# Kernel tuning notes

Measured on AMD Instinct MI355X. Metric: run time of the kernel, lower is better.

Reference implementation:

```python
import jax, jax.numpy as jnp
import numpy as np

N_NODES = 50000
N_EDGES = 800000
F_IN = 128
HID = 128
HID4 = HID // 4  # 32
N_SEL = 8192


def gcn_conv(x, src, dst, norm, W, b, n_nodes):
    h = x @ W                              # [N, out]
    msg = h[src] * norm[:, None]           # gather + scale, [E+N, out]
    out = jax.ops.segment_sum(msg, dst, num_segments=n_nodes)  # scatter-add
    return out + b


def setup_inputs() -> dict:
    key = jax.random.key(0)
    ks = jax.random.split(key, 12)
    def glorot(k, shape):
        lim = np.sqrt(6.0 / (shape[0] + shape[1])).astype(np.float32)
        return jax.random.uniform(k, shape, jnp.float32, -lim, lim)
    return {
        "x": jax.random.normal(ks[0], (N_NODES, F_IN), jnp.float32),
        "edge_index": jax.random.randint(ks[1], (2, N_EDGES), 0, N_NODES, jnp.int64 if jax.config.jax_enable_x64 else jnp.int32),
        "relevant_batch_indices": jax.random.randint(ks[2], (N_SEL,), 0, N_NODES),
        "labels": jax.random.randint(ks[3], (N_SEL,), 0, 2),
        "W1": glorot(ks[4], (F_IN, HID)),   "b1": jnp.zeros((HID,), jnp.float32),
        "W2": glorot(ks[5], (HID, HID4)),   "b2": jnp.zeros((HID4,), jnp.float32),
        "W3": glorot(ks[6], (HID4, HID4)),  "b3": jnp.zeros((HID4,), jnp.float32),
        "Wl": glorot(ks[7], (HID4, 2)),     "bl": jnp.zeros((2,), jnp.float32),
    }


def reference(x, edge_index, relevant_batch_indices, labels, W1, b1, W2, b2, W3, b3, Wl, bl):
    n = x.shape[0]
    loops = jnp.arange(n, dtype=edge_index.dtype)
    src = jnp.concatenate([edge_index[0], loops])  # add self-loops
    dst = jnp.concatenate([edge_index[1], loops])
    deg = jax.ops.segment_sum(jnp.ones_like(dst, dtype=x.dtype), dst, num_segments=n)
    dis = jnp.where(deg > 0, jax.lax.rsqrt(jnp.maximum(deg, 1e-12)), 0.0)
    norm = dis[src] * dis[dst]             # [E+N]

    h = jax.nn.relu(gcn_conv(x, src, dst, norm, W1, b1, n))
    h = jax.nn.relu(gcn_conv(h, src, dst, norm, W2, b2, n))
    h = gcn_conv(h, src, dst, norm, W3, b3, n)

    logits = h[relevant_batch_indices] @ Wl + bl   # [N_SEL, 2]
    softmax_vals = jax.nn.softmax(logits, axis=1)
    lsm = jax.nn.log_softmax(logits, axis=1)
    # original slices lsm to labels length if longer; here shapes match
    lsm = lsm[: labels.shape[0]]
    return (lsm, softmax_vals)
```

## Files before the change

### kernel.cpp

```cpp
#include <hip/hip_runtime.h>
#include <hip/hip_fp16.h>

#define F_IN 128
#define HID 128
#define HID4 32
#define NPB 256
#define SRC_BITS 17
#define NBK 256
#define MAXBUCKET 256

static inline size_t alignup(size_t x) { return (x + 255) & ~(size_t)255; }

typedef _Float16 half8 __attribute__((ext_vector_type(8)));
typedef float f32x4 __attribute__((ext_vector_type(4)));

union F4H8 { float4 f; __half2 h[4]; };
union U2H4 { uint2 u; _Float16 h[4]; };


__global__ __launch_bounds__(1024) void hist_k(const int* __restrict__ dst,
                                               int* __restrict__ ghist,
                                               const float* __restrict__ W1,
                                               _Float16* __restrict__ Wt,
                                               int ne, int n_buckets) {
    __shared__ int h[MAXBUCKET];
    const int t = threadIdx.x;
    if (blockIdx.x < 16) {
        int q = blockIdx.x * 1024 + t;
        int k = q >> 7, n = q & 127;
        Wt[n * 128 + k] = (_Float16)W1[q];
    }
    for (int b = t; b < n_buckets; b += 1024) h[b] = 0;
    __syncthreads();
    const int chunk = (ne + NBK - 1) / NBK;
    const int beg = blockIdx.x * chunk;
    const int end = min(ne, beg + chunk);
    for (int e = beg + t; e < end; e += 1024)
        atomicAdd(&h[dst[e] / NPB], 1);
    __syncthreads();
    for (int b = t; b < n_buckets; b += 1024)
        ghist[(size_t)b * NBK + blockIdx.x] = h[b];
}


__global__ void scan_block_k(const int* __restrict__ in, int* __restrict__ out,
                             int* __restrict__ partials, int n) {
    __shared__ int tmp[256];
    int i = blockIdx.x * 256 + threadIdx.x;
    int v = (i < n) ? in[i] : 0;
    tmp[threadIdx.x] = v;
    __syncthreads();
    for (int off = 1; off < 256; off <<= 1) {
        int t = (threadIdx.x >= off) ? tmp[threadIdx.x - off] : 0;
        __syncthreads();
        tmp[threadIdx.x] += t;
        __syncthreads();
    }
    if (i < n) out[i] = tmp[threadIdx.x] - v;
    if (threadIdx.x == 255) partials[blockIdx.x] = tmp[255];
}

__global__ void scan_partials_k(int* __restrict__ partials, int nb) {
    __shared__ int tmp[256];
    int v = (threadIdx.x < nb) ? partials[threadIdx.x] : 0;
    tmp[threadIdx.x] = v;
    __syncthreads();
    for (int off = 1; off < 256; off <<= 1) {
        int t = (threadIdx.x >= off) ? tmp[threadIdx.x - off] : 0;
        __syncthreads();
        tmp[threadIdx.x] += t;
        __syncthreads();
    }
    if (threadIdx.x < nb) partials[threadIdx.x] = tmp[threadIdx.x] - v;
}


__global__ __launch_bounds__(1024) void scatter2_k(const int* __restrict__ src, const int* __restrict__ dst,
                                                   const int* __restrict__ goff,
                                                   const int* __restrict__ partial2,
                                                   unsigned* __restrict__ tmp, int ne, int n_buckets) {
    __shared__ int cur[MAXBUCKET];
    const int t = threadIdx.x;
    for (int b = t; b < n_buckets; b += 1024)
        cur[b] = goff[(size_t)b * NBK + blockIdx.x] + partial2[b];
    __syncthreads();
    const int chunk = (ne + NBK - 1) / NBK;
    const int beg = blockIdx.x * chunk;
    const int end = min(ne, beg + chunk);
    for (int e = beg + t; e < end; e += 1024) {
        int d = dst[e];
        int s = src[e];
        int pos = atomicAdd(&cur[d / NPB], 1);
        tmp[pos] = ((unsigned)(d & (NPB - 1)) << SRC_BITS) | (unsigned)s;
    }
}


__global__ __launch_bounds__(NPB) void binC_k(const unsigned* __restrict__ tmp,
                                              const int* __restrict__ goff,
                                              const int* __restrict__ partial2,
                                              int* __restrict__ deg, float* __restrict__ dis,
                                              int* __restrict__ rowoff, int* __restrict__ csr,
                                              int* __restrict__ order,
                                              int n_nodes, int ne, int n_buckets) {
    __shared__ int cnt[NPB];
    __shared__ int sc[NPB];
    __shared__ int dh[64];
    __shared__ int db[64];
    const int t = threadIdx.x;
    const int bid = blockIdx.x;
    const int base = goff[(size_t)bid * NBK] + partial2[bid];
    const int end = (bid + 1 < n_buckets) ? goff[(size_t)(bid + 1) * NBK] + partial2[bid + 1] : ne;

    cnt[t] = 0;
    if (t < 64) dh[t] = 0;
    __syncthreads();
    for (int j = base + t; j < end; j += NPB)
        atomicAdd(&cnt[tmp[j] >> SRC_BITS], 1);
    __syncthreads();

    int mydeg = cnt[t];
    sc[t] = mydeg;
    __syncthreads();
    for (int off = 1; off < NPB; off <<= 1) {
        int v = (t >= off) ? sc[t - off] : 0;
        __syncthreads();
        sc[t] += v;
        __syncthreads();
    }
    int excl = sc[t] - mydeg;
    int node = bid * NPB + t;
    const bool valid = node < n_nodes;
    if (valid) {
        deg[node] = mydeg;
        dis[node] = rsqrtf((float)(mydeg + 1));
        rowoff[node] = base + excl;
    }
    cnt[t] = base + excl;

    int bin = min(mydeg, 63);
    if (valid) atomicAdd(&dh[bin], 1);
    __syncthreads();
    if (t == 0) {
        int run = 0;
        #pragma unroll
        for (int i = 0; i < 64; ++i) { db[i] = run; run += dh[i]; }
    }
    __syncthreads();
    if (valid) {
        int rank = atomicAdd(&db[bin], 1);
        order[bid * NPB + rank] = node;
    }

    for (int j = base + t; j < end; j += NPB) {
        unsigned e = tmp[j];
        int ld = e >> SRC_BITS;
        int s  = e & ((1u << SRC_BITS) - 1);
        int pos = atomicAdd(&cnt[ld], 1);
        csr[pos] = s;
    }
}


__global__ __launch_bounds__(256) void gemm1_mfma_k(const float* __restrict__ in,
                                                    const _Float16* __restrict__ Wt,
                                                    const float* __restrict__ dis,
                                                    __half* __restrict__ hout, int n_rows) {
    __shared__ _Float16 xs[64][136];
    const int t = threadIdx.x;
    const int row0 = blockIdx.x * 64;

    #pragma unroll
    for (int i = 0; i < 8; ++i) {
        int q = t + i * 256;
        int row = q >> 5, c4 = (q & 31) * 4;
        float4 v = make_float4(0.f, 0.f, 0.f, 0.f);
        if (row0 + row < n_rows) v = *(const float4*)(in + (size_t)(row0 + row) * 128 + c4);
        U2H4 cv;
        cv.h[0] = (_Float16)v.x; cv.h[1] = (_Float16)v.y;
        cv.h[2] = (_Float16)v.z; cv.h[3] = (_Float16)v.w;
        *(uint2*)&xs[row][c4] = cv.u;
    }
    __syncthreads();

    const int lane = t & 63;
    const int wave = t >> 6;
    const int r0 = wave * 16;
    const int lrow = lane & 15;
    const int kgrp = (lane >> 4) * 8;

    f32x4 acc[8];
    #pragma unroll
    for (int c = 0; c < 8; ++c) acc[c] = (f32x4){0.f, 0.f, 0.f, 0.f};

    #pragma unroll
    for (int kk = 0; kk < 4; ++kk) {
        const int k0 = kk * 32 + kgrp;
        half8 a = *(const half8*)&xs[r0 + lrow][k0];
        #pragma unroll
        for (int ct = 0; ct < 8; ++ct) {
            half8 b = *(const half8*)(Wt + (size_t)(ct * 16 + lrow) * 128 + k0);
            acc[ct] = __builtin_amdgcn_mfma_f32_16x16x32_f16(a, b, acc[ct], 0, 0, 0);
        }
    }

    const int rbase = row0 + r0 + (lane >> 4) * 4;
    #pragma unroll
    for (int i = 0; i < 4; ++i) {
        int row = rbase + i;
        if (row < n_rows) {
            float sc = dis[row];
            __half* p = hout + (size_t)row * 128 + lrow;
            #pragma unroll
            for (int ct = 0; ct < 8; ++ct)
                p[ct * 16] = __float2half(sc * acc[ct][i]);
        }
    }
}


__global__ void pull1_k(const __half* __restrict__ g, const int* __restrict__ rowoff,
                        const int* __restrict__ deg, const int* __restrict__ csr,
                        const int* __restrict__ order,
                        const float* __restrict__ dis, const float* __restrict__ b,
                        __half* __restrict__ out, int n_nodes) {
    int gt = blockIdx.x * blockDim.x + threadIdx.x;
    int idx = gt >> 4;
    int f0 = (gt & 15) * 8;
    if (idx >= n_nodes) return;
    int node = order[idx];
    int beg = rowoff[node];
    int end = beg + deg[node];
    float dd = dis[node];

    float acc[8];
    {
        F4H8 v; v.f = *(const float4*)(g + (size_t)node * 128 + f0);
        #pragma unroll
        for (int k = 0; k < 4; ++k) {
            float2 p = __half22float2(v.h[k]);
            acc[2 * k] = p.x; acc[2 * k + 1] = p.y;
        }
    }

    int j = beg;
    for (; j + 2 <= end; j += 2) {
        int s0 = csr[j];
        int s1 = csr[j + 1];
        F4H8 v0; v0.f = *(const float4*)(g + (size_t)s0 * 128 + f0);
        F4H8 v1; v1.f = *(const float4*)(g + (size_t)s1 * 128 + f0);
        #pragma unroll
        for (int k = 0; k < 4; ++k) {
            float2 p0 = __half22float2(v0.h[k]);
            float2 p1 = __half22float2(v1.h[k]);
            acc[2 * k]     += p0.x + p1.x;
            acc[2 * k + 1] += p0.y + p1.y;
        }
    }
    if (j < end) {
        int s = csr[j];
        F4H8 v; v.f = *(const float4*)(g + (size_t)s * 128 + f0);
        #pragma unroll
        for (int k = 0; k < 4; ++k) {
            float2 p = __half22float2(v.h[k]);
            acc[2 * k] += p.x; acc[2 * k + 1] += p.y;
        }
    }

    float4 b0 = *(const float4*)(b + f0);
    float4 b1 = *(const float4*)(b + f0 + 4);
    F4H8 o;
    o.h[0] = __floats2half2_rn(fmaxf(b0.x + dd * acc[0], 0.f), fmaxf(b0.y + dd * acc[1], 0.f));
    o.h[1] = __floats2half2_rn(fmaxf(b0.z + dd * acc[2], 0.f), fmaxf(b0.w + dd * acc[3], 0.f));
    o.h[2] = __floats2half2_rn(fmaxf(b1.x + dd * acc[4], 0.f), fmaxf(b1.y + dd * acc[5], 0.f));
    o.h[3] = __floats2half2_rn(fmaxf(b1.z + dd * acc[6], 0.f), fmaxf(b1.w + dd * acc[7], 0.f));
    *(float4*)(out + (size_t)node * 128 + f0) = o.f;
}


__global__ __launch_bounds__(256) void gemm2_k(const __half* __restrict__ in,
                                               const float* __restrict__ W,
                                               const float* __restrict__ dis,
                                               __half* __restrict__ out, int n_rows) {
    __shared__ float xs[64][132];
    __shared__ float wt[128][32];
    const int t = threadIdx.x;
    const int row0 = blockIdx.x * 64;

    #pragma unroll
    for (int i = 0; i < 4; ++i) {
        int q = t + i * 256;
        int row = q >> 4, c8 = (q & 15) * 8;
        F4H8 v;
        v.f = make_float4(0.f, 0.f, 0.f, 0.f);
        if (row0 + row < n_rows)
            v.f = *(const float4*)(in + (size_t)(row0 + row) * 128 + c8);
        #pragma unroll
        for (int k = 0; k < 4; ++k) {
            float2 p = __half22float2(v.h[k]);
            xs[row][c8 + 2 * k] = p.x;
            xs[row][c8 + 2 * k + 1] = p.y;
        }
    }
    #pragma unroll
    for (int i = 0; i < 4; ++i) {
        int q = t + i * 256;
        int kk = q >> 3, c4 = (q & 7) * 4;
        *(float4*)&wt[kk][c4] = *(const float4*)(W + (size_t)kk * 32 + c4);
    }
    __syncthreads();

    const int c4 = (t & 7) * 4;
    const int r2 = (t >> 3) * 2;

    float acc[2][4];
    #pragma unroll
    for (int i = 0; i < 2; ++i)
        #pragma unroll
        for (int j = 0; j < 4; ++j) acc[i][j] = 0.f;

    #pragma unroll 4
    for (int k = 0; k < 128; ++k) {
        float x0 = xs[r2][k], x1 = xs[r2 + 1][k];
        float4 w = *(float4*)&wt[k][c4];
        acc[0][0] += x0 * w.x; acc[0][1] += x0 * w.y; acc[0][2] += x0 * w.z; acc[0][3] += x0 * w.w;
        acc[1][0] += x1 * w.x; acc[1][1] += x1 * w.y; acc[1][2] += x1 * w.z; acc[1][3] += x1 * w.w;
    }

    #pragma unroll
    for (int i = 0; i < 2; ++i) {
        int row = row0 + r2 + i;
        if (row < n_rows) {
            float sc = dis[row];
            U2H4 cv;
            cv.h[0] = (_Float16)(sc * acc[i][0]);
            cv.h[1] = (_Float16)(sc * acc[i][1]);
            cv.h[2] = (_Float16)(sc * acc[i][2]);
            cv.h[3] = (_Float16)(sc * acc[i][3]);
            *(uint2*)(out + (size_t)row * 32 + c4) = cv.u;
        }
    }
}


__global__ void pull2_k(const __half* __restrict__ g, const int* __restrict__ rowoff,
                        const int* __restrict__ deg, const int* __restrict__ csr,
                        const int* __restrict__ order,
                        const float* __restrict__ dis, const float* __restrict__ b,
                        float* __restrict__ out, int n_nodes) {
    int gt = blockIdx.x * blockDim.x + threadIdx.x;
    int idx = gt >> 3;
    int f0 = (gt & 7) * 4;
    if (idx >= n_nodes) return;
    int node = order[idx];
    int beg = rowoff[node];
    int end = beg + deg[node];
    float dd = dis[node];

    float acc[4];
    {
        U2H4 v; v.u = *(const uint2*)(g + (size_t)node * 32 + f0);
        #pragma unroll
        for (int k = 0; k < 4; ++k) acc[k] = (float)v.h[k];
    }

    int j = beg;
    for (; j + 2 <= end; j += 2) {
        int s0 = csr[j];
        int s1 = csr[j + 1];
        U2H4 v0; v0.u = *(const uint2*)(g + (size_t)s0 * 32 + f0);
        U2H4 v1; v1.u = *(const uint2*)(g + (size_t)s1 * 32 + f0);
        #pragma unroll
        for (int k = 0; k < 4; ++k) acc[k] += (float)v0.h[k] + (float)v1.h[k];
    }
    if (j < end) {
        int s = csr[j];
        U2H4 v; v.u = *(const uint2*)(g + (size_t)s * 32 + f0);
        #pragma unroll
        for (int k = 0; k < 4; ++k) acc[k] += (float)v.h[k];
    }

    float4 bb = *(const float4*)(b + f0);
    *(float4*)(out + (size_t)node * 32 + f0) =
        make_float4(bb.x + dd * acc[0], bb.y + dd * acc[1],
                    bb.z + dd * acc[2], bb.w + dd * acc[3]);
}


__global__ __launch_bounds__(256) void gemm3_k(const float* __restrict__ in,
                                               const float* __restrict__ W,
                                               const float* __restrict__ dis,
                                               float* __restrict__ out, int n_rows) {
    __shared__ float xs[64][36];
    __shared__ float wt[32][32];
    const int t = threadIdx.x;
    const int row0 = blockIdx.x * 64;

    #pragma unroll
    for (int i = 0; i < 2; ++i) {
        int q = t + i * 256;
        int row = q >> 3, c4 = (q & 7) * 4;
        float4 v = make_float4(0.f, 0.f, 0.f, 0.f);
        if (row0 + row < n_rows) {
            v = *(const float4*)(in + (size_t)(row0 + row) * 32 + c4);
            v.x = fmaxf(v.x, 0.f); v.y = fmaxf(v.y, 0.f);
            v.z = fmaxf(v.z, 0.f); v.w = fmaxf(v.w, 0.f);
        }
        *(float4*)&xs[row][c4] = v;
    }
    {
        int kk = t >> 3, c4 = (t & 7) * 4;
        *(float4*)&wt[kk][c4] = *(const float4*)(W + (size_t)kk * 32 + c4);
    }
    __syncthreads();

    const int c4 = (t & 7) * 4;
    const int r2 = (t >> 3) * 2;

    float acc[2][4];
    #pragma unroll
    for (int i = 0; i < 2; ++i)
        #pragma unroll
        for (int j = 0; j < 4; ++j) acc[i][j] = 0.f;

    #pragma unroll
    for (int k = 0; k < 32; ++k) {
        float x0 = xs[r2][k], x1 = xs[r2 + 1][k];
        float4 w = *(float4*)&wt[k][c4];
        acc[0][0] += x0 * w.x; acc[0][1] += x0 * w.y; acc[0][2] += x0 * w.z; acc[0][3] += x0 * w.w;
        acc[1][0] += x1 * w.x; acc[1][1] += x1 * w.y; acc[1][2] += x1 * w.z; acc[1][3] += x1 * w.w;
    }

    #pragma unroll
    for (int i = 0; i < 2; ++i) {
        int row = row0 + r2 + i;
        if (row < n_rows) {
            float sc = dis[row];
            *(float4*)(out + (size_t)row * 32 + c4) =
                make_float4(sc * acc[i][0], sc * acc[i][1], sc * acc[i][2], sc * acc[i][3]);
        }
    }
}


__global__ void pull_head_k(const float* __restrict__ g, const int* __restrict__ rowoff,
                            const int* __restrict__ deg, const int* __restrict__ csr,
                            const float* __restrict__ dis, const float* __restrict__ b3,
                            const int* __restrict__ sel, const float* __restrict__ Wl,
                            const float* __restrict__ bl, float* __restrict__ out, int n_sel) {
    int gt = blockIdx.x * blockDim.x + threadIdx.x;
    int t = gt >> 3;
    int f0 = (gt & 7) * 4;
    if (t >= n_sel) return;
    int node = sel[t];
    int beg = rowoff[node];
    int end = beg + deg[node];
    float dd = dis[node];

    float4 acc = *(const float4*)(g + (size_t)node * 32 + f0);

    int j = beg;
    for (; j + 2 <= end; j += 2) {
        int s0 = csr[j];
        int s1 = csr[j + 1];
        float4 h0 = *(const float4*)(g + (size_t)s0 * 32 + f0);
        float4 h1 = *(const float4*)(g + (size_t)s1 * 32 + f0);
        acc.x += h0.x + h1.x;
        acc.y += h0.y + h1.y;
        acc.z += h0.z + h1.z;
        acc.w += h0.w + h1.w;
    }
    if (j < end) {
        int s = csr[j];
        float4 hs = *(const float4*)(g + (size_t)s * 32 + f0);
        acc.x += hs.x; acc.y += hs.y; acc.z += hs.z; acc.w += hs.w;
    }

    float4 bb = *(const float4*)(b3 + f0);
    float a0 = bb.x + dd * acc.x;
    float a1 = bb.y + dd * acc.y;
    float a2 = bb.z + dd * acc.z;
    float a3 = bb.w + dd * acc.w;

    float l0 = a0 * Wl[(f0 + 0) * 2] + a1 * Wl[(f0 + 1) * 2]
             + a2 * Wl[(f0 + 2) * 2] + a3 * Wl[(f0 + 3) * 2];
    float l1 = a0 * Wl[(f0 + 0) * 2 + 1] + a1 * Wl[(f0 + 1) * 2 + 1]
             + a2 * Wl[(f0 + 2) * 2 + 1] + a3 * Wl[(f0 + 3) * 2 + 1];
    #pragma unroll
    for (int m = 1; m < 8; m <<= 1) {
        l0 += __shfl_xor(l0, m);
        l1 += __shfl_xor(l1, m);
    }
    if ((gt & 7) == 0) {
        l0 += bl[0]; l1 += bl[1];
        float mx = fmaxf(l0, l1);
        float e0 = expf(l0 - mx), e1 = expf(l1 - mx);
        float s = e0 + e1;
        float ls = logf(s);
        *(float2*)(out + (size_t)t * 2) = make_float2((l0 - mx) - ls, (l1 - mx) - ls);
        *(float2*)(out + 2 * (size_t)n_sel + (size_t)t * 2) = make_float2(e0 / s, e1 / s);
    }
}


extern "C" void kernel_launch(void* const* d_in, const int* in_sizes, int n_in,
                              void* d_out, int out_size, void* d_ws, size_t ws_size,
                              hipStream_t stream) {
    const float* x  = (const float*)d_in[0];
    const int* edge = (const int*)d_in[1];
    const int* sel  = (const int*)d_in[2];
    const float* W1 = (const float*)d_in[4];
    const float* b1 = (const float*)d_in[5];
    const float* W2 = (const float*)d_in[6];
    const float* b2 = (const float*)d_in[7];
    const float* W3 = (const float*)d_in[8];
    const float* b3 = (const float*)d_in[9];
    const float* Wl = (const float*)d_in[10];
    const float* bl = (const float*)d_in[11];
    float* out = (float*)d_out;

    const int n_nodes = in_sizes[0] / F_IN;
    const int n_edges = in_sizes[1] / 2;
    const int n_sel   = in_sizes[2];
    const int* srcv = edge;
    const int* dstv = edge + n_edges;
    const int n_buckets = (n_nodes + NPB - 1) / NPB;
    const int n_gh = n_buckets * NBK;

    char* ws = (char*)d_ws;
    int*       deg      = (int*)ws;       ws += alignup((size_t)n_nodes * 4);
    float*     dis      = (float*)ws;     ws += alignup((size_t)n_nodes * 4);
    int*       rowoff   = (int*)ws;       ws += alignup((size_t)n_nodes * 4);
    int*       order    = (int*)ws;       ws += alignup((size_t)n_nodes * 4);
    int*       ghist    = (int*)ws;       ws += alignup((size_t)n_gh * 4);
    int*       goff     = (int*)ws;       ws += alignup((size_t)n_gh * 4);
    int*       partial2 = (int*)ws;       ws += alignup(1024);
    _Float16*  Wt       = (_Float16*)ws;  ws += alignup(128 * 128 * 2);
    unsigned*  tmp      = (unsigned*)ws;  ws += alignup((size_t)n_edges * 4);
    int*       csr      = (int*)ws;       ws += alignup((size_t)n_edges * 4);
    char*      bufA     = ws;             ws += alignup((size_t)n_nodes * HID * 4);
    char*      bufB     = ws;

    const int B = 256;
    #define GRD(n) (((n) + B - 1) / B)
    const int nblk2 = GRD(n_gh);

    hist_k<<<NBK, 1024, 0, stream>>>(dstv, ghist, W1, Wt, n_edges, n_buckets);
    scan_block_k<<<nblk2, B, 0, stream>>>(ghist, goff, partial2, n_gh);
    scan_partials_k<<<1, B, 0, stream>>>(partial2, nblk2);
    scatter2_k<<<NBK, 1024, 0, stream>>>(srcv, dstv, goff, partial2, tmp, n_edges, n_buckets);
    binC_k<<<n_buckets, NPB, 0, stream>>>(tmp, goff, partial2, deg, dis, rowoff, csr, order,
                                          n_nodes, n_edges, n_buckets);

    const int gemm_blocks = (n_nodes + 63) / 64;

    gemm1_mfma_k<<<gemm_blocks, B, 0, stream>>>(x, Wt, dis, (__half*)bufA, n_nodes);
    pull1_k<<<GRD(n_nodes * 16), B, 0, stream>>>((const __half*)bufA, rowoff, deg, csr, order,
                                                 dis, b1, (__half*)bufB, n_nodes);

    gemm2_k<<<gemm_blocks, B, 0, stream>>>((const __half*)bufB, W2, dis, (__half*)bufA, n_nodes);
    pull2_k<<<GRD(n_nodes * 8), B, 0, stream>>>((const __half*)bufA, rowoff, deg, csr, order,
                                                dis, b2, (float*)bufB, n_nodes);

    gemm3_k<<<gemm_blocks, B, 0, stream>>>((const float*)bufB, W3, dis, (float*)bufA, n_nodes);
    pull_head_k<<<GRD(n_sel * 8), B, 0, stream>>>((const float*)bufA, rowoff, deg, csr, dis, b3,
                                                  sel, Wl, bl, out, n_sel);

    #undef GRD
}
```

Baseline: 141.5 us.

## Fuse edge scatter with layer-1 GEMM and drop degree-sorted node ordering

The first-layer GEMM no longer pre-scales rows by the source degree norm. That lets it run in the same launch as the edge scatter, with extra blocks past the scatter blocks doing the MFMA GEMM using 1024 threads (16 waves, each computing 32 columns). The source-side norm is instead applied per edge in pull1 by loading dis[s] for each neighbor. The degree-histogram ordering of nodes in binC and the order indirection in pull1/pull2 are removed, so nodes are processed in natural order. This trades an extra per-edge dis load and lost degree-balanced scheduling for one fewer launch and overlap of the GEMM with the scatter.

```diff
diff --git a/kernel.cpp b/kernel.cpp
--- a/kernel.cpp
+++ b/kernel.cpp
@@ -75,104 +75,37 @@
 }
 
 
-__global__ __launch_bounds__(1024) void scatter2_k(const int* __restrict__ src, const int* __restrict__ dst,
-                                                   const int* __restrict__ goff,
-                                                   const int* __restrict__ partial2,
-                                                   unsigned* __restrict__ tmp, int ne, int n_buckets) {
+__global__ __launch_bounds__(1024) void fused_scatter_gemm1_k(
+        const int* __restrict__ src, const int* __restrict__ dst,
+        const int* __restrict__ goff, const int* __restrict__ partial2,
+        unsigned* __restrict__ tmp, int ne, int n_buckets,
+        const float* __restrict__ in, const _Float16* __restrict__ Wt,
+        __half* __restrict__ hout, int n_rows) {
     __shared__ int cur[MAXBUCKET];
-    const int t = threadIdx.x;
-    for (int b = t; b < n_buckets; b += 1024)
-        cur[b] = goff[(size_t)b * NBK + blockIdx.x] + partial2[b];
-    __syncthreads();
-    const int chunk = (ne + NBK - 1) / NBK;
-    const int beg = blockIdx.x * chunk;
-    const int end = min(ne, beg + chunk);
-    for (int e = beg + t; e < end; e += 1024) {
-        int d = dst[e];
-        int s = src[e];
-        int pos = atomicAdd(&cur[d / NPB], 1);
-        tmp[pos] = ((unsigned)(d & (NPB - 1)) << SRC_BITS) | (unsigned)s;
-    }
-}
-
-
-__global__ __launch_bounds__(NPB) void binC_k(const unsigned* __restrict__ tmp,
-                                              const int* __restrict__ goff,
-                                              const int* __restrict__ partial2,
-                                              int* __restrict__ deg, float* __restrict__ dis,
-                                              int* __restrict__ rowoff, int* __restrict__ csr,
-                                              int* __restrict__ order,
-                                              int n_nodes, int ne, int n_buckets) {
-    __shared__ int cnt[NPB];
-    __shared__ int sc[NPB];
-    __shared__ int dh[64];
-    __shared__ int db[64];
-    const int t = threadIdx.x;
-    const int bid = blockIdx.x;
-    const int base = goff[(size_t)bid * NBK] + partial2[bid];
-    const int end = (bid + 1 < n_buckets) ? goff[(size_t)(bid + 1) * NBK] + partial2[bid + 1] : ne;
-
-    cnt[t] = 0;
-    if (t < 64) dh[t] = 0;
-    __syncthreads();
-    for (int j = base + t; j < end; j += NPB)
-        atomicAdd(&cnt[tmp[j] >> SRC_BITS], 1);
-    __syncthreads();
-
-    int mydeg = cnt[t];
-    sc[t] = mydeg;
-    __syncthreads();
-    for (int off = 1; off < NPB; off <<= 1) {
-        int v = (t >= off) ? sc[t - off] : 0;
-        __syncthreads();
-        sc[t] += v;
-        __syncthreads();
-    }
-    int excl = sc[t] - mydeg;
-    int node = bid * NPB + t;
-    const bool valid = node < n_nodes;
-    if (valid) {
-        deg[node] = mydeg;
-        dis[node] = rsqrtf((float)(mydeg + 1));
-        rowoff[node] = base + excl;
-    }
-    cnt[t] = base + excl;
-
-    int bin = min(mydeg, 63);
-    if (valid) atomicAdd(&dh[bin], 1);
-    __syncthreads();
-    if (t == 0) {
-        int run = 0;
-        #pragma unroll
-        for (int i = 0; i < 64; ++i) { db[i] = run; run += dh[i]; }
-    }
-    __syncthreads();
-    if (valid) {
-        int rank = atomicAdd(&db[bin], 1);
-        order[bid * NPB + rank] = node;
-    }
-
-    for (int j = base + t; j < end; j += NPB) {
-        unsigned e = tmp[j];
-        int ld = e >> SRC_BITS;
-        int s  = e & ((1u << SRC_BITS) - 1);
-        int pos = atomicAdd(&cnt[ld], 1);
-        csr[pos] = s;
-    }
-}
-
-
-__global__ __launch_bounds__(256) void gemm1_mfma_k(const float* __restrict__ in,
-                                                    const _Float16* __restrict__ Wt,
-                                                    const float* __restrict__ dis,
-                                                    __half* __restrict__ hout, int n_rows) {
     __shared__ _Float16 xs[64][136];
     const int t = threadIdx.x;
-    const int row0 = blockIdx.x * 64;
-
-    #pragma unroll
-    for (int i = 0; i < 8; ++i) {
-        int q = t + i * 256;
+
+    if (blockIdx.x < NBK) {
+        for (int b = t; b < n_buckets; b += 1024)
+            cur[b] = goff[(size_t)b * NBK + blockIdx.x] + partial2[b];
+        __syncthreads();
+        const int chunk = (ne + NBK - 1) / NBK;
+        const int beg = blockIdx.x * chunk;
+        const int end = min(ne, beg + chunk);
+        for (int e = beg + t; e < end; e += 1024) {
+            int d = dst[e];
+            int s = src[e];
+            int pos = atomicAdd(&cur[d / NPB], 1);
+            tmp[pos] = ((unsigned)(d & (NPB - 1)) << SRC_BITS) | (unsigned)s;
+        }
+        return;
+    }
+
+    const int row0 = (blockIdx.x - NBK) * 64;
+
+    #pragma unroll
+    for (int i = 0; i < 2; ++i) {
+        int q = t + i * 1024;
         int row = q >> 5, c4 = (q & 31) * 4;
         float4 v = make_float4(0.f, 0.f, 0.f, 0.f);
         if (row0 + row < n_rows) v = *(const float4*)(in + (size_t)(row0 + row) * 128 + c4);
@@ -185,21 +118,22 @@
 
     const int lane = t & 63;
     const int wave = t >> 6;
-    const int r0 = wave * 16;
+    const int r0 = (wave & 3) * 16;
+    const int cg = (wave >> 2) * 32;
     const int lrow = lane & 15;
     const int kgrp = (lane >> 4) * 8;
 
-    f32x4 acc[8];
-    #pragma unroll
-    for (int c = 0; c < 8; ++c) acc[c] = (f32x4){0.f, 0.f, 0.f, 0.f};
+    f32x4 acc[2];
+    acc[0] = (f32x4){0.f, 0.f, 0.f, 0.f};
+    acc[1] = (f32x4){0.f, 0.f, 0.f, 0.f};
 
     #pragma unroll
     for (int kk = 0; kk < 4; ++kk) {
         const int k0 = kk * 32 + kgrp;
         half8 a = *(const half8*)&xs[r0 + lrow][k0];
         #pragma unroll
-        for (int ct = 0; ct < 8; ++ct) {
-            half8 b = *(const half8*)(Wt + (size_t)(ct * 16 + lrow) * 128 + k0);
+        for (int ct = 0; ct < 2; ++ct) {
+            half8 b = *(const half8*)(Wt + (size_t)(cg + ct * 16 + lrow) * 128 + k0);
             acc[ct] = __builtin_amdgcn_mfma_f32_16x16x32_f16(a, b, acc[ct], 0, 0, 0);
         }
     }
@@ -207,28 +141,72 @@
     const int rbase = row0 + r0 + (lane >> 4) * 4;
     #pragma unroll
     for (int i = 0; i < 4; ++i) {
-        int row = rbase + i;
+        int row = row0 + r0 + (lane >> 4) * 4 + i;
         if (row < n_rows) {
-            float sc = dis[row];
-            __half* p = hout + (size_t)row * 128 + lrow;
-            #pragma unroll
-            for (int ct = 0; ct < 8; ++ct)
-                p[ct * 16] = __float2half(sc * acc[ct][i]);
-        }
+            __half* p = hout + (size_t)row * 128 + cg + lrow;
+            p[0]  = __float2half(acc[0][i]);
+            p[16] = __float2half(acc[1][i]);
+        }
+    }
+    (void)rbase;
+}
+
+
+__global__ __launch_bounds__(NPB) void binC_k(const unsigned* __restrict__ tmp,
+                                              const int* __restrict__ goff,
+                                              const int* __restrict__ partial2,
+                                              int* __restrict__ deg, float* __restrict__ dis,
+                                              int* __restrict__ rowoff, int* __restrict__ csr,
+                                              int n_nodes, int ne, int n_buckets) {
+    __shared__ int cnt[NPB];
+    __shared__ int sc[NPB];
+    const int t = threadIdx.x;
+    const int bid = blockIdx.x;
+    const int base = goff[(size_t)bid * NBK] + partial2[bid];
+    const int end = (bid + 1 < n_buckets) ? goff[(size_t)(bid + 1) * NBK] + partial2[bid + 1] : ne;
+
+    cnt[t] = 0;
+    __syncthreads();
+    for (int j = base + t; j < end; j += NPB)
+        atomicAdd(&cnt[tmp[j] >> SRC_BITS], 1);
+    __syncthreads();
+
+    int mydeg = cnt[t];
+    sc[t] = mydeg;
+    __syncthreads();
+    for (int off = 1; off < NPB; off <<= 1) {
+        int v = (t >= off) ? sc[t - off] : 0;
+        __syncthreads();
+        sc[t] += v;
+        __syncthreads();
+    }
+    int excl = sc[t] - mydeg;
+    int node = bid * NPB + t;
+    if (node < n_nodes) {
+        deg[node] = mydeg;
+        dis[node] = rsqrtf((float)(mydeg + 1));
+        rowoff[node] = base + excl;
+    }
+    cnt[t] = base + excl;
+    __syncthreads();
+    for (int j = base + t; j < end; j += NPB) {
+        unsigned e = tmp[j];
+        int ld = e >> SRC_BITS;
+        int s  = e & ((1u << SRC_BITS) - 1);
+        int pos = atomicAdd(&cnt[ld], 1);
+        csr[pos] = s;
     }
 }
 
 
 __global__ void pull1_k(const __half* __restrict__ g, const int* __restrict__ rowoff,
                         const int* __restrict__ deg, const int* __restrict__ csr,
-                        const int* __restrict__ order,
                         const float* __restrict__ dis, const float* __restrict__ b,
                         __half* __restrict__ out, int n_nodes) {
     int gt = blockIdx.x * blockDim.x + threadIdx.x;
-    int idx = gt >> 4;
+    int node = gt >> 4;
     int f0 = (gt & 15) * 8;
-    if (idx >= n_nodes) return;
-    int node = order[idx];
+    if (node >= n_nodes) return;
     int beg = rowoff[node];
     int end = beg + deg[node];
     float dd = dis[node];
@@ -239,7 +217,7 @@
         #pragma unroll
         for (int k = 0; k < 4; ++k) {
             float2 p = __half22float2(v.h[k]);
-            acc[2 * k] = p.x; acc[2 * k + 1] = p.y;
+            acc[2 * k] = dd * p.x; acc[2 * k + 1] = dd * p.y;
         }
     }
 
@@ -247,23 +225,26 @@
     for (; j + 2 <= end; j += 2) {
         int s0 = csr[j];
         int s1 = csr[j + 1];
+        float w0 = dis[s0];
+        float w1 = dis[s1];
         F4H8 v0; v0.f = *(const float4*)(g + (size_t)s0 * 128 + f0);
         F4H8 v1; v1.f = *(const float4*)(g + (size_t)s1 * 128 + f0);
         #pragma unroll
         for (int k = 0; k < 4; ++k) {
             float2 p0 = __half22float2(v0.h[k]);
             float2 p1 = __half22float2(v1.h[k]);
-            acc[2 * k]     += p0.x + p1.x;
-            acc[2 * k + 1] += p0.y + p1.y;
+            acc[2 * k]     += w0 * p0.x + w1 * p1.x;
+            acc[2 * k + 1] += w0 * p0.y + w1 * p1.y;
         }
     }
     if (j < end) {
         int s = csr[j];
+        float w = dis[s];
         F4H8 v; v.f = *(const float4*)(g + (size_t)s * 128 + f0);
         #pragma unroll
         for (int k = 0; k < 4; ++k) {
             float2 p = __half22float2(v.h[k]);
-            acc[2 * k] += p.x; acc[2 * k + 1] += p.y;
+            acc[2 * k] += w * p.x; acc[2 * k + 1] += w * p.y;
         }
     }
 
@@ -345,14 +326,12 @@
 
 __global__ void pull2_k(const __half* __restrict__ g, const int* __restrict__ rowoff,
                         const int* __restrict__ deg, const int* __restrict__ csr,
-                        const int* __restrict__ order,
                         const float* __restrict__ dis, const float* __restrict__ b,
                         float* __restrict__ out, int n_nodes) {
     int gt = blockIdx.x * blockDim.x + threadIdx.x;
-    int idx = gt >> 3;
+    int node = gt >> 3;
     int f0 = (gt & 7) * 4;
-    if (idx >= n_nodes) return;
-    int node = order[idx];
+    if (node >= n_nodes) return;
     int beg = rowoff[node];
     int end = beg + deg[node];
     float dd = dis[node];
@@ -531,7 +510,6 @@
     int*       deg      = (int*)ws;       ws += alignup((size_t)n_nodes * 4);
     float*     dis      = (float*)ws;     ws += alignup((size_t)n_nodes * 4);
     int*       rowoff   = (int*)ws;       ws += alignup((size_t)n_nodes * 4);
-    int*       order    = (int*)ws;       ws += alignup((size_t)n_nodes * 4);
     int*       ghist    = (int*)ws;       ws += alignup((size_t)n_gh * 4);
     int*       goff     = (int*)ws;       ws += alignup((size_t)n_gh * 4);
     int*       partial2 = (int*)ws;       ws += alignup(1024);
@@ -544,22 +522,24 @@
     const int B = 256;
     #define GRD(n) (((n) + B - 1) / B)
     const int nblk2 = GRD(n_gh);
+    const int gemm_blocks = (n_nodes + 63) / 64;
 
     hist_k<<<NBK, 1024, 0, stream>>>(dstv, ghist, W1, Wt, n_edges, n_buckets);
     scan_block_k<<<nblk2, B, 0, stream>>>(ghist, goff, partial2, n_gh);
     scan_partials_k<<<1, B, 0, stream>>>(partial2, nblk2);
-    scatter2_k<<<NBK, 1024, 0, stream>>>(srcv, dstv, goff, partial2, tmp, n_edges, n_buckets);
-    binC_k<<<n_buckets, NPB, 0, stream>>>(tmp, goff, partial2, deg, dis, rowoff, csr, order,
+
+    fused_scatter_gemm1_k<<<NBK + gemm_blocks, 1024, 0, stream>>>(
+        srcv, dstv, goff, partial2, tmp, n_edges, n_buckets,
+        x, Wt, (__half*)bufA, n_nodes);
+
+    binC_k<<<n_buckets, NPB, 0, stream>>>(tmp, goff, partial2, deg, dis, rowoff, csr,
                                           n_nodes, n_edges, n_buckets);
 
-    const int gemm_blocks = (n_nodes + 63) / 64;
-
-    gemm1_mfma_k<<<gemm_blocks, B, 0, stream>>>(x, Wt, dis, (__half*)bufA, n_nodes);
-    pull1_k<<<GRD(n_nodes * 16), B, 0, stream>>>((const __half*)bufA, rowoff, deg, csr, order,
+    pull1_k<<<GRD(n_nodes * 16), B, 0, stream>>>((const __half*)bufA, rowoff, deg, csr,
                                                  dis, b1, (__half*)bufB, n_nodes);
 
     gemm2_k<<<gemm_blocks, B, 0, stream>>>((const __half*)bufB, W2, dis, (__half*)bufA, n_nodes);
-    pull2_k<<<GRD(n_nodes * 8), B, 0, stream>>>((const __half*)bufA, rowoff, deg, csr, order,
+    pull2_k<<<GRD(n_nodes * 8), B, 0, stream>>>((const __half*)bufA, rowoff, deg, csr,
                                                 dis, b2, (float*)bufB, n_nodes);
 
     gemm3_k<<<gemm_blocks, B, 0, stream>>>((const float*)bufB, W3, dis, (float*)bufA, n_nodes);
```

New measurement: 129.3 us. -8.6%, faster.
